# Optimization experiments

Measured on AMD Instinct MI355X. Metric: run time of the kernel, lower is better.

Reference implementation:

```python
import jax, jax.numpy as jnp
import numpy as np

EMBED_DIM, NUM_HEADS, WINDOW_SIZE, IS_REVERSE = 192, 6, 7, False
B, H, W = 2, 56, 56


def toodd(s):
    return s if s % 2 == 1 else s + 1


def window_start(length, K, dilation):
    # NATTEN-style clamped neighborhood start indices (static, numpy)
    NS = K // 2
    idx = np.arange(length)
    if dilation <= 1:
        return np.maximum(idx - NS, 0) + np.where(idx + NS >= length, length - idx - NS - 1, 0)
    ni = idx - NS * dilation
    imodd = idx % dilation
    a = (length // dilation) * dilation
    b = length - a
    end_start = np.where(imodd < b, length - b + imodd - 2 * NS * dilation, a + imodd - K * dilation)
    return np.where(ni < 0, imodd, np.where(idx + NS * dilation >= length, end_start, ni))


def na2d(q, k, v, K, dilation):
    # q,k,v: (b, n, H, W, d); returns attended v, same shape
    b, n, h, w, d = q.shape
    ih = window_start(h, K, dilation)[:, None] + np.arange(K) * dilation  # (H, K)
    iw = window_start(w, K, dilation)[:, None] + np.arange(K) * dilation  # (W, K)
    kg = k[:, :, ih][:, :, :, :, iw]  # (b,n,H,K,W,K,d)
    attn = jnp.einsum('bnhwd,bnhpwqd->bnhwpq', q, kg)
    attn = jax.nn.softmax(attn.reshape(b, n, h, w, K * K), axis=-1).reshape(b, n, h, w, K, K)
    vg = v[:, :, ih][:, :, :, :, iw]  # (b,n,H,K,W,K,d)
    return jnp.einsum('bnhwpq,bnhpwqd->bnhwd', attn, vg)


def setup_inputs() -> dict:
    key = jax.random.key(0)
    ks = jax.random.split(key, 7)
    E = EMBED_DIM
    return {
        'x': jax.random.normal(ks[0], (B, E, H, W), jnp.float32),
        'qkv_w': jax.random.normal(ks[1], (3 * E, E, 1, 1), jnp.float32) * 0.02,
        'qkv_b': jax.random.normal(ks[2], (3 * E,), jnp.float32) * 0.02,
        'lepe_w': jax.random.normal(ks[3], (E, 1, 5, 5), jnp.float32) * 0.02,
        'lepe_b': jax.random.normal(ks[4], (E,), jnp.float32) * 0.02,
        'out_w': jax.random.normal(ks[5], (E, E, 1, 1), jnp.float32) * 0.02,
        'out_b': jnp.zeros((E,), jnp.float32),
    }


def reference(x, qkv_w, qkv_b, lepe_w, lepe_b, out_w, out_b):
    E, n = EMBED_DIM, NUM_HEADS
    b, _, h, w = x.shape
    d = E // n
    scaling = d ** -0.5
    # 1x1 conv qkv
    qkv = jnp.einsum('bchw,oc->bohw', x, qkv_w[:, :, 0, 0]) + qkv_b[None, :, None, None]
    # depthwise 5x5 LePE on the v channels
    lepe = jax.lax.conv_general_dilated(
        qkv[:, 2 * E:], lepe_w, (1, 1), ((2, 2), (2, 2)),
        feature_group_count=E, dimension_numbers=('NCHW', 'OIHW', 'NCHW')
    ) + lepe_b[None, :, None, None]
    # rearrange 'b (m n d) h w -> m b n h w d'
    qkv = qkv.reshape(b, 3, n, d, h, w)
    q = jnp.transpose(qkv[:, 0], (0, 1, 3, 4, 2))
    k = jnp.transpose(qkv[:, 1], (0, 1, 3, 4, 2)) * scaling
    v = jnp.transpose(qkv[:, 2], (0, 1, 3, 4, 2))
    if not IS_REVERSE:
        ws, gs = WINDOW_SIZE, min(h, w) // WINDOW_SIZE
    else:
        gs, ws = WINDOW_SIZE, min(h, w) // WINDOW_SIZE
    if ws > 1:
        v = na2d(q, k, v, toodd(ws), 1)
    if gs > 1:
        stride = ws
        while toodd(gs) * stride > min(h, w):
            stride -= 1
        v = na2d(q, k, v, toodd(gs), stride)
    res = jnp.transpose(v, (0, 1, 4, 2, 3)).reshape(b, E, h, w) + lepe
    return jnp.einsum('bchw,oc->bohw', res, out_w[:, :, 0, 0]) + out_b[None, :, None, None]
```

## Files before the change

### kernel.cpp

```cpp
#include <hip/hip_runtime.h>

#define BATCH 2
#define EDIM 192
#define NHEAD 6
#define DHEAD 32
#define HH 56
#define WW 56
#define NPIX (HH * WW)

__device__ __forceinline__ int win_start(int i, int length, int K, int dil) {
    int NS = K >> 1;
    if (dil <= 1) {
        int s = i - NS;
        if (s < 0) s = 0;
        if (i + NS >= length) s += length - i - NS - 1;
        return s;
    }
    int ni = i - NS * dil;
    int imodd = i % dil;
    int aa = (length / dil) * dil;
    int bb = length - aa;
    int end_start = (imodd < bb) ? (length - bb + imodd - 2 * NS * dil)
                                 : (aa + imodd - K * dil);
    if (ni < 0) return imodd;
    if (i + NS * dil >= length) return end_start;
    return ni;
}

#define DOT4(a, b) ((a).x * (b).x + (a).y * (b).y + (a).z * (b).z + (a).w * (b).w)


__global__ __launch_bounds__(256) void qkv_conv_kernel(
    const float* __restrict__ x, const float* __restrict__ w,
    const float* __restrict__ bias,
    float* __restrict__ q_pm, float* __restrict__ k_pm,
    float* __restrict__ v_pm, float* __restrict__ v_cm)
{
    __shared__ float red[4][8][256];
    const int b  = blockIdx.z;
    const int o0 = blockIdx.y * 8;
    const int p0 = blockIdx.x * 256;
    const int wv = threadIdx.x >> 6;
    const int lane = threadIdx.x & 63;

    int pix[4];
#pragma unroll
    for (int j = 0; j < 4; ++j) {
        int p = p0 + lane + j * 64;
        pix[j] = p < NPIX ? p : NPIX - 1;
    }
    const float* xb = x + (size_t)b * EDIM * NPIX;
    const float* wb = w + (size_t)o0 * EDIM;

    float acc[8][4];
#pragma unroll
    for (int o = 0; o < 8; ++o)
#pragma unroll
        for (int j = 0; j < 4; ++j) acc[o][j] = 0.f;

    const int c0 = wv * 48;
    for (int c = c0; c < c0 + 48; c += 4) {
        float4 wr[8];
#pragma unroll
        for (int o = 0; o < 8; ++o)
            wr[o] = *reinterpret_cast<const float4*>(wb + o * EDIM + c);
        float xv[4][4];
#pragma unroll
        for (int i = 0; i < 4; ++i) {
            const float* xc = xb + (size_t)(c + i) * NPIX;
#pragma unroll
            for (int j = 0; j < 4; ++j) xv[i][j] = xc[pix[j]];
        }
#pragma unroll
        for (int o = 0; o < 8; ++o)
#pragma unroll
            for (int j = 0; j < 4; ++j) {
                float a = acc[o][j];
                a = fmaf(xv[0][j], wr[o].x, a);
                a = fmaf(xv[1][j], wr[o].y, a);
                a = fmaf(xv[2][j], wr[o].z, a);
                a = fmaf(xv[3][j], wr[o].w, a);
                acc[o][j] = a;
            }
    }
#pragma unroll
    for (int o = 0; o < 8; ++o)
#pragma unroll
        for (int j = 0; j < 4; ++j) red[wv][o][lane + j * 64] = acc[o][j];
    __syncthreads();

    const int p = threadIdx.x;
    const int gp = p0 + p;
    if (gp >= NPIX) return;
    float vals[8];
#pragma unroll
    for (int o = 0; o < 8; ++o)
        vals[o] = red[0][o][p] + red[1][o][p] + red[2][o][p] + red[3][o][p]
                + bias[o0 + o];

    const int m  = o0 / EDIM;
    const int hd = (o0 % EDIM) / DHEAD;
    const int d0 = o0 % DHEAD;
    float* pm = (m == 0 ? q_pm : (m == 1 ? k_pm : v_pm));
    if (m == 1) {
        const float ks = 0.17677669529663687f;
#pragma unroll
        for (int o = 0; o < 8; ++o) vals[o] *= ks;
    }
    float* dst = pm + ((size_t)(b * NHEAD + hd) * NPIX + gp) * DHEAD + d0;
    *reinterpret_cast<float4*>(dst)     = make_float4(vals[0], vals[1], vals[2], vals[3]);
    *reinterpret_cast<float4*>(dst + 4) = make_float4(vals[4], vals[5], vals[6], vals[7]);
    if (m == 2) {
        float* vc = v_cm + ((size_t)b * EDIM + hd * DHEAD + d0) * NPIX + gp;
#pragma unroll
        for (int o = 0; o < 8; ++o) vc[(size_t)o * NPIX] = vals[o];
    }
}

__global__ __launch_bounds__(256) void out_conv_kernel(
    const float* __restrict__ v2, const float* __restrict__ lepe,
    const float* __restrict__ w, const float* __restrict__ bias,
    float* __restrict__ out)
{
    __shared__ float red[4][8][256];
    const int b  = blockIdx.z;
    const int o0 = blockIdx.y * 8;
    const int p0 = blockIdx.x * 256;
    const int wv = threadIdx.x >> 6;
    const int lane = threadIdx.x & 63;

    int pix[4];
#pragma unroll
    for (int j = 0; j < 4; ++j) {
        int p = p0 + lane + j * 64;
        pix[j] = p < NPIX ? p : NPIX - 1;
    }
    const float* vb = v2   + (size_t)b * EDIM * NPIX;
    const float* lb = lepe + (size_t)b * EDIM * NPIX;
    const float* wb = w + (size_t)o0 * EDIM;

    float acc[8][4];
#pragma unroll
    for (int o = 0; o < 8; ++o)
#pragma unroll
        for (int j = 0; j < 4; ++j) acc[o][j] = 0.f;

    const int c0 = wv * 48;
    for (int c = c0; c < c0 + 48; c += 4) {
        float4 wr[8];
#pragma unroll
        for (int o = 0; o < 8; ++o)
            wr[o] = *reinterpret_cast<const float4*>(wb + o * EDIM + c);
        float xv[4][4];
#pragma unroll
        for (int i = 0; i < 4; ++i) {
            const float* vc = vb + (size_t)(c + i) * NPIX;
            const float* lc = lb + (size_t)(c + i) * NPIX;
#pragma unroll
            for (int j = 0; j < 4; ++j) xv[i][j] = vc[pix[j]] + lc[pix[j]];
        }
#pragma unroll
        for (int o = 0; o < 8; ++o)
#pragma unroll
            for (int j = 0; j < 4; ++j) {
                float a = acc[o][j];
                a = fmaf(xv[0][j], wr[o].x, a);
                a = fmaf(xv[1][j], wr[o].y, a);
                a = fmaf(xv[2][j], wr[o].z, a);
                a = fmaf(xv[3][j], wr[o].w, a);
                acc[o][j] = a;
            }
    }
#pragma unroll
    for (int o = 0; o < 8; ++o)
#pragma unroll
        for (int j = 0; j < 4; ++j) red[wv][o][lane + j * 64] = acc[o][j];
    __syncthreads();

    const int p = threadIdx.x;
    const int gp = p0 + p;
    if (gp >= NPIX) return;
#pragma unroll
    for (int o = 0; o < 8; ++o) {
        const float val = red[0][o][p] + red[1][o][p] + red[2][o][p] + red[3][o][p]
                        + bias[o0 + o];
        out[((size_t)b * EDIM + o0 + o) * NPIX + gp] = val;
    }
}

__global__ __launch_bounds__(256) void lepe_kernel(
    const float* __restrict__ v_cm, const float* __restrict__ w,
    const float* __restrict__ bias, float* __restrict__ out)
{
    const int t = blockIdx.x * 256 + threadIdx.x;
    if (t >= BATCH * EDIM * NPIX) return;
    const int yx = t % NPIX;
    const int bc = t / NPIX;
    const int c = bc % EDIM;
    const int y = yx / WW, x = yx % WW;

    const float* vp = v_cm + (size_t)bc * NPIX;
    const float* wp = w + (size_t)c * 25;
    float acc = bias[c];
#pragma unroll
    for (int dy = 0; dy < 5; ++dy) {
        const int yy = y + dy - 2;
        if (yy < 0 || yy >= HH) continue;
#pragma unroll
        for (int dx = 0; dx < 5; ++dx) {
            const int xx = x + dx - 2;
            if (xx < 0 || xx >= WW) continue;
            acc = fmaf(vp[yy * WW + xx], wp[dy * 5 + dx], acc);
        }
    }
    out[t] = acc;
}

template<int K, int DIL, bool OUT_CM>
__global__ __launch_bounds__(256) void na2d_kernel(
    const float* __restrict__ q, const float* __restrict__ k,
    const float* __restrict__ v, float* __restrict__ out)
{
    const int tid  = blockIdx.x * 256 + threadIdx.x;
    const int lane = threadIdx.x & 63;
    const int dg   = lane & 7;
    const int qs   = lane >> 3;
    const int qid  = (tid >> 6) * 8 + qs;
    const int yx = qid % NPIX;
    const int bn = qid / NPIX;
    const int y = yx / WW, x = yx % WW;
    const int ys = win_start(y, HH, K, DIL);
    const int xs = win_start(x, WW, K, DIL);

    const float4 qr = *reinterpret_cast<const float4*>(
        q + ((size_t)bn * NPIX + yx) * DHEAD + dg * 4);
    const float* kb = k + (size_t)bn * NPIX * DHEAD + dg * 4;
    const float* vb = v + (size_t)bn * NPIX * DHEAD + dg * 4;

    float m = -3.0e38f, s = 0.f;
    float4 o = make_float4(0.f, 0.f, 0.f, 0.f);

    for (int r = 0; r < K; ++r) {
        const int rowpix = (ys + r * DIL) * WW + xs;
        const float* krow = kb + (size_t)rowpix * DHEAD;
        const float* vrow = vb + (size_t)rowpix * DHEAD;
        float4 kbuf[K], vbuf[K];
#pragma unroll
        for (int c = 0; c < K; ++c)
            kbuf[c] = *reinterpret_cast<const float4*>(krow + c * (DIL * DHEAD));
#pragma unroll
        for (int c = 0; c < K; ++c)
            vbuf[c] = *reinterpret_cast<const float4*>(vrow + c * (DIL * DHEAD));

        float sc[K];
#pragma unroll
        for (int c = 0; c < K; ++c) {
            float d = DOT4(kbuf[c], qr);
            d += __shfl_xor(d, 1);
            d += __shfl_xor(d, 2);
            d += __shfl_xor(d, 4);
            sc[c] = d;
        }
        float rm = sc[0];
#pragma unroll
        for (int c = 1; c < K; ++c) rm = fmaxf(rm, sc[c]);
        const float nm = fmaxf(m, rm);
        const float alpha = __expf(m - nm);
        s *= alpha;
        o.x *= alpha; o.y *= alpha; o.z *= alpha; o.w *= alpha;
        m = nm;
#pragma unroll
        for (int c = 0; c < K; ++c) {
            const float wgt = __expf(sc[c] - m);
            s += wgt;
            o.x = fmaf(wgt, vbuf[c].x, o.x);
            o.y = fmaf(wgt, vbuf[c].y, o.y);
            o.z = fmaf(wgt, vbuf[c].z, o.z);
            o.w = fmaf(wgt, vbuf[c].w, o.w);
        }
    }
    const float inv = 1.f / s;
    o.x *= inv; o.y *= inv; o.z *= inv; o.w *= inv;
    if (OUT_CM) {
        float* op = out + ((size_t)bn * DHEAD + dg * 4) * NPIX + yx;
        op[0] = o.x; op[NPIX] = o.y; op[2 * NPIX] = o.z; op[3 * NPIX] = o.w;
    } else {
        *reinterpret_cast<float4*>(
            out + ((size_t)bn * NPIX + yx) * DHEAD + dg * 4) = o;
    }
}

extern "C" void kernel_launch(void* const* d_in, const int* in_sizes, int n_in,
                              void* d_out, int out_size, void* d_ws, size_t ws_size,
                              hipStream_t stream)
{
    const float* x      = (const float*)d_in[0];
    const float* qkv_w  = (const float*)d_in[1];
    const float* qkv_b  = (const float*)d_in[2];
    const float* lepe_w = (const float*)d_in[3];
    const float* lepe_b = (const float*)d_in[4];
    const float* out_w  = (const float*)d_in[5];
    const float* out_b  = (const float*)d_in[6];
    float* out = (float*)d_out;

    const size_t ESZ = (size_t)BATCH * EDIM * NPIX;
    float* ws   = (float*)d_ws;
    float* q_pm = ws;
    float* k_pm = q_pm + ESZ;
    float* v_pm = k_pm + ESZ;
    float* v_cm = v_pm + ESZ;
    float* lepe = v_cm + ESZ;
    float* v1   = lepe + ESZ;
    float* v2   = v_pm;

    const int ptiles = (NPIX + 255) / 256;

    dim3 gq(ptiles, (3 * EDIM) / 8, BATCH);
    qkv_conv_kernel<<<gq, 256, 0, stream>>>(x, qkv_w, qkv_b, q_pm, k_pm, v_pm, v_cm);

    const int lepe_threads = BATCH * EDIM * NPIX;
    lepe_kernel<<<(lepe_threads + 255) / 256, 256, 0, stream>>>(v_cm, lepe_w, lepe_b, lepe);

    const int attn_blocks = (BATCH * NHEAD * NPIX * 8) / 256;
    na2d_kernel<7, 1, false><<<attn_blocks, 256, 0, stream>>>(q_pm, k_pm, v_pm, v1);

    na2d_kernel<9, 6, true><<<attn_blocks, 256, 0, stream>>>(q_pm, k_pm, v1, v2);

    dim3 go(ptiles, EDIM / 8, BATCH);
    out_conv_kernel<<<go, 256, 0, stream>>>(v2, lepe, out_w, out_b, out);
}
```

Baseline: 137.9 us.

## Restructure 1x1 conv kernels: full-K per thread, float2 pixels, register double-buffering

Both the qkv and output 1x1 convolution kernels drop the four-wave channel split and its shared-memory reduction. Each thread now covers all 192 input channels for two adjacent pixels, using float2 loads and double-buffered register prefetch of inputs and weights. The grid is reordered so output-channel blocks vary fastest, which lets blocks sharing a pixel tile hit L2 for x. This removes the LDS reduction and barrier, but halves the block count and lengthens each thread's serial chain, which may reduce latency hiding.

New measurement: 139.8 us. No clear change (+1.4%).

```diff
diff --git a/kernel.cpp b/kernel.cpp
--- a/kernel.cpp
+++ b/kernel.cpp
@@ -30,90 +30,87 @@
 #define DOT4(a, b) ((a).x * (b).x + (a).y * (b).y + (a).z * (b).z + (a).w * (b).w)
 
 
+#define CONV_FMA(XV, WV)                                     \
+    _Pragma("unroll")                                        \
+    for (int o = 0; o < 8; ++o) {                            \
+        acc[o][0] = fmaf(XV[0].x, WV[o].x, acc[o][0]);       \
+        acc[o][1] = fmaf(XV[0].y, WV[o].x, acc[o][1]);       \
+        acc[o][0] = fmaf(XV[1].x, WV[o].y, acc[o][0]);       \
+        acc[o][1] = fmaf(XV[1].y, WV[o].y, acc[o][1]);       \
+        acc[o][0] = fmaf(XV[2].x, WV[o].z, acc[o][0]);       \
+        acc[o][1] = fmaf(XV[2].y, WV[o].z, acc[o][1]);       \
+        acc[o][0] = fmaf(XV[3].x, WV[o].w, acc[o][0]);       \
+        acc[o][1] = fmaf(XV[3].y, WV[o].w, acc[o][1]);       \
+    }
+
 __global__ __launch_bounds__(256) void qkv_conv_kernel(
     const float* __restrict__ x, const float* __restrict__ w,
     const float* __restrict__ bias,
     float* __restrict__ q_pm, float* __restrict__ k_pm,
     float* __restrict__ v_pm, float* __restrict__ v_cm)
 {
-    __shared__ float red[4][8][256];
     const int b  = blockIdx.z;
-    const int o0 = blockIdx.y * 8;
-    const int p0 = blockIdx.x * 256;
-    const int wv = threadIdx.x >> 6;
-    const int lane = threadIdx.x & 63;
-
-    int pix[4];
-#pragma unroll
-    for (int j = 0; j < 4; ++j) {
-        int p = p0 + lane + j * 64;
-        pix[j] = p < NPIX ? p : NPIX - 1;
-    }
-    const float* xb = x + (size_t)b * EDIM * NPIX;
+    const int o0 = blockIdx.x * 8;
+    const int p0 = blockIdx.y * 512;
+    int pb = p0 + threadIdx.x * 2;
+    if (pb > NPIX - 2) pb = NPIX - 2;
+    const float* xb = x + (size_t)b * EDIM * NPIX + pb;
     const float* wb = w + (size_t)o0 * EDIM;
 
-    float acc[8][4];
+    float acc[8][2];
+#pragma unroll
+    for (int o = 0; o < 8; ++o) { acc[o][0] = 0.f; acc[o][1] = 0.f; }
+
+    float2 xA[4], xB[4];
+    float4 wA[8], wB[8];
+#pragma unroll
+    for (int i = 0; i < 4; ++i)
+        xA[i] = *reinterpret_cast<const float2*>(xb + (size_t)i * NPIX);
 #pragma unroll
     for (int o = 0; o < 8; ++o)
-#pragma unroll
-        for (int j = 0; j < 4; ++j) acc[o][j] = 0.f;
-
-    const int c0 = wv * 48;
-    for (int c = c0; c < c0 + 48; c += 4) {
-        float4 wr[8];
+        wA[o] = *reinterpret_cast<const float4*>(wb + o * EDIM);
+
+    for (int c = 0; c < EDIM; c += 8) {
+#pragma unroll
+        for (int i = 0; i < 4; ++i)
+            xB[i] = *reinterpret_cast<const float2*>(xb + (size_t)(c + 4 + i) * NPIX);
 #pragma unroll
         for (int o = 0; o < 8; ++o)
-            wr[o] = *reinterpret_cast<const float4*>(wb + o * EDIM + c);
-        float xv[4][4];
-#pragma unroll
-        for (int i = 0; i < 4; ++i) {
-            const float* xc = xb + (size_t)(c + i) * NPIX;
-#pragma unroll
-            for (int j = 0; j < 4; ++j) xv[i][j] = xc[pix[j]];
-        }
-#pragma unroll
-        for (int o = 0; o < 8; ++o)
-#pragma unroll
-            for (int j = 0; j < 4; ++j) {
-                float a = acc[o][j];
-                a = fmaf(xv[0][j], wr[o].x, a);
-                a = fmaf(xv[1][j], wr[o].y, a);
-                a = fmaf(xv[2][j], wr[o].z, a);
-                a = fmaf(xv[3][j], wr[o].w, a);
-                acc[o][j] = a;
-            }
-    }
-#pragma unroll
-    for (int o = 0; o < 8; ++o)
-#pragma unroll
-        for (int j = 0; j < 4; ++j) red[wv][o][lane + j * 64] = acc[o][j];
-    __syncthreads();
-
-    const int p = threadIdx.x;
-    const int gp = p0 + p;
-    if (gp >= NPIX) return;
-    float vals[8];
-#pragma unroll
-    for (int o = 0; o < 8; ++o)
-        vals[o] = red[0][o][p] + red[1][o][p] + red[2][o][p] + red[3][o][p]
-                + bias[o0 + o];
+            wB[o] = *reinterpret_cast<const float4*>(wb + o * EDIM + c + 4);
+        CONV_FMA(xA, wA);
+        if (c + 8 < EDIM) {
+#pragma unroll
+            for (int i = 0; i < 4; ++i)
+                xA[i] = *reinterpret_cast<const float2*>(xb + (size_t)(c + 8 + i) * NPIX);
+#pragma unroll
+            for (int o = 0; o < 8; ++o)
+                wA[o] = *reinterpret_cast<const float4*>(wb + o * EDIM + c + 8);
+        }
+        CONV_FMA(xB, wB);
+    }
 
     const int m  = o0 / EDIM;
     const int hd = (o0 % EDIM) / DHEAD;
     const int d0 = o0 % DHEAD;
     float* pm = (m == 0 ? q_pm : (m == 1 ? k_pm : v_pm));
-    if (m == 1) {
-        const float ks = 0.17677669529663687f;
-#pragma unroll
-        for (int o = 0; o < 8; ++o) vals[o] *= ks;
-    }
-    float* dst = pm + ((size_t)(b * NHEAD + hd) * NPIX + gp) * DHEAD + d0;
-    *reinterpret_cast<float4*>(dst)     = make_float4(vals[0], vals[1], vals[2], vals[3]);
-    *reinterpret_cast<float4*>(dst + 4) = make_float4(vals[4], vals[5], vals[6], vals[7]);
-    if (m == 2) {
-        float* vc = v_cm + ((size_t)b * EDIM + hd * DHEAD + d0) * NPIX + gp;
-#pragma unroll
-        for (int o = 0; o < 8; ++o) vc[(size_t)o * NPIX] = vals[o];
+    const float ks = (m == 1) ? 0.17677669529663687f : 1.f;
+
+#pragma unroll
+    for (int j = 0; j < 2; ++j) {
+        const int gp = p0 + threadIdx.x * 2 + j;
+        if (gp >= NPIX) continue;
+        float vals[8];
+#pragma unroll
+        for (int o = 0; o < 8; ++o)
+            vals[o] = (acc[o][j] + bias[o0 + o]) * ks;
+        float* dst = pm + ((size_t)(b * NHEAD + hd) * NPIX + gp) * DHEAD + d0;
+        *reinterpret_cast<float4*>(dst)     = make_float4(vals[0], vals[1], vals[2], vals[3]);
+        *reinterpret_cast<float4*>(dst + 4) = make_float4(vals[4], vals[5], vals[6], vals[7]);
+        if (m == 2) {
+            float* vc = v_cm + ((size_t)b * EDIM + hd * DHEAD + d0) * NPIX + gp;
+#pragma unroll
+            for (int o = 0; o < 8; ++o) vc[(size_t)o * NPIX] = vals[o];
+        }
     }
 }
 
@@ -122,69 +119,63 @@
     const float* __restrict__ w, const float* __restrict__ bias,
     float* __restrict__ out)
 {
-    __shared__ float red[4][8][256];
     const int b  = blockIdx.z;
-    const int o0 = blockIdx.y * 8;
-    const int p0 = blockIdx.x * 256;
-    const int wv = threadIdx.x >> 6;
-    const int lane = threadIdx.x & 63;
-
-    int pix[4];
-#pragma unroll
-    for (int j = 0; j < 4; ++j) {
-        int p = p0 + lane + j * 64;
-        pix[j] = p < NPIX ? p : NPIX - 1;
-    }
-    const float* vb = v2   + (size_t)b * EDIM * NPIX;
-    const float* lb = lepe + (size_t)b * EDIM * NPIX;
+    const int o0 = blockIdx.x * 8;
+    const int p0 = blockIdx.y * 512;
+    int pb = p0 + threadIdx.x * 2;
+    if (pb > NPIX - 2) pb = NPIX - 2;
+    const float* vb = v2   + (size_t)b * EDIM * NPIX + pb;
+    const float* lb = lepe + (size_t)b * EDIM * NPIX + pb;
     const float* wb = w + (size_t)o0 * EDIM;
 
-    float acc[8][4];
+    float acc[8][2];
+#pragma unroll
+    for (int o = 0; o < 8; ++o) { acc[o][0] = 0.f; acc[o][1] = 0.f; }
+
+    float2 xA[4], xB[4];
+    float4 wA[8], wB[8];
+#pragma unroll
+    for (int i = 0; i < 4; ++i) {
+        const float2 v0 = *reinterpret_cast<const float2*>(vb + (size_t)i * NPIX);
+        const float2 l0 = *reinterpret_cast<const float2*>(lb + (size_t)i * NPIX);
+        xA[i] = make_float2(v0.x + l0.x, v0.y + l0.y);
+    }
 #pragma unroll
     for (int o = 0; o < 8; ++o)
-#pragma unroll
-        for (int j = 0; j < 4; ++j) acc[o][j] = 0.f;
-
-    const int c0 = wv * 48;
-    for (int c = c0; c < c0 + 48; c += 4) {
-        float4 wr[8];
+        wA[o] = *reinterpret_cast<const float4*>(wb + o * EDIM);
+
+    for (int c = 0; c < EDIM; c += 8) {
+#pragma unroll
+        for (int i = 0; i < 4; ++i) {
+            const float2 v0 = *reinterpret_cast<const float2*>(vb + (size_t)(c + 4 + i) * NPIX);
+            const float2 l0 = *reinterpret_cast<const float2*>(lb + (size_t)(c + 4 + i) * NPIX);
+            xB[i] = make_float2(v0.x + l0.x, v0.y + l0.y);
+        }
 #pragma unroll
         for (int o = 0; o < 8; ++o)
-            wr[o] = *reinterpret_cast<const float4*>(wb + o * EDIM + c);
-        float xv[4][4];
-#pragma unroll
-        for (int i = 0; i < 4; ++i) {
-            const float* vc = vb + (size_t)(c + i) * NPIX;
-            const float* lc = lb + (size_t)(c + i) * NPIX;
-#pragma unroll
-            for (int j = 0; j < 4; ++j) xv[i][j] = vc[pix[j]] + lc[pix[j]];
-        }
+            wB[o] = *reinterpret_cast<const float4*>(wb + o * EDIM + c + 4);
+        CONV_FMA(xA, wA);
+        if (c + 8 < EDIM) {
+#pragma unroll
+            for (int i = 0; i < 4; ++i) {
+                const float2 v0 = *reinterpret_cast<const float2*>(vb + (size_t)(c + 8 + i) * NPIX);
+                const float2 l0 = *reinterpret_cast<const float2*>(lb + (size_t)(c + 8 + i) * NPIX);
+                xA[i] = make_float2(v0.x + l0.x, v0.y + l0.y);
+            }
+#pragma unroll
+            for (int o = 0; o < 8; ++o)
+                wA[o] = *reinterpret_cast<const float4*>(wb + o * EDIM + c + 8);
+        }
+        CONV_FMA(xB, wB);
+    }
+
+#pragma unroll
+    for (int j = 0; j < 2; ++j) {
+        const int gp = p0 + threadIdx.x * 2 + j;
+        if (gp >= NPIX) continue;
 #pragma unroll
         for (int o = 0; o < 8; ++o)
-#pragma unroll
-            for (int j = 0; j < 4; ++j) {
-                float a = acc[o][j];
-                a = fmaf(xv[0][j], wr[o].x, a);
-                a = fmaf(xv[1][j], wr[o].y, a);
-                a = fmaf(xv[2][j], wr[o].z, a);
-                a = fmaf(xv[3][j], wr[o].w, a);
-                acc[o][j] = a;
-            }
-    }
-#pragma unroll
-    for (int o = 0; o < 8; ++o)
-#pragma unroll
-        for (int j = 0; j < 4; ++j) red[wv][o][lane + j * 64] = acc[o][j];
-    __syncthreads();
-
-    const int p = threadIdx.x;
-    const int gp = p0 + p;
-    if (gp >= NPIX) return;
-#pragma unroll
-    for (int o = 0; o < 8; ++o) {
-        const float val = red[0][o][p] + red[1][o][p] + red[2][o][p] + red[3][o][p]
-                        + bias[o0 + o];
-        out[((size_t)b * EDIM + o0 + o) * NPIX + gp] = val;
+            out[((size_t)b * EDIM + o0 + o) * NPIX + gp] = acc[o][j] + bias[o0 + o];
     }
 }
 
@@ -313,9 +304,9 @@
     float* v1   = lepe + ESZ;
     float* v2   = v_pm;
 
-    const int ptiles = (NPIX + 255) / 256;
-
-    dim3 gq(ptiles, (3 * EDIM) / 8, BATCH);
+    const int ptiles = (NPIX + 511) / 512;
+
+    dim3 gq((3 * EDIM) / 8, ptiles, BATCH);
     qkv_conv_kernel<<<gq, 256, 0, stream>>>(x, qkv_w, qkv_b, q_pm, k_pm, v_pm, v_cm);
 
     const int lepe_threads = BATCH * EDIM * NPIX;
@@ -326,6 +317,6 @@
 
     na2d_kernel<9, 6, true><<<attn_blocks, 256, 0, stream>>>(q_pm, k_pm, v1, v2);
 
-    dim3 go(ptiles, EDIM / 8, BATCH);
+    dim3 go(EDIM / 8, ptiles, BATCH);
     out_conv_kernel<<<go, 256, 0, stream>>>(v2, lepe, out_w, out_b, out);
 }
```
